# Kernel optimization log

Measured on AMD Instinct MI355X. Metric: run time of the kernel, lower is better.

The kernel has to match this reference:

```python
import jax, jax.numpy as jnp
import numpy as np

T, B, IN_DIM, MEM_DIM = 512, 64, 512, 512


def _kaiming(key, shape):
    fan_in = shape[1]
    return jax.random.normal(key, shape, dtype=jnp.float32) * np.sqrt(2.0 / fan_in)


def setup_inputs() -> dict:
    key = jax.random.key(0)
    ks = jax.random.split(key, 5)
    return {
        "inputs": jax.random.normal(ks[0], (T, B, IN_DIM), dtype=jnp.float32),
        "h0": jnp.zeros((B, MEM_DIM), dtype=jnp.float32),
        "c0": jnp.zeros((B, MEM_DIM), dtype=jnp.float32),
        "W_ioux": _kaiming(ks[1], (3 * MEM_DIM, IN_DIM)),
        "b_ioux": jnp.zeros((3 * MEM_DIM,), dtype=jnp.float32),
        "W_iouh": _kaiming(ks[2], (3 * MEM_DIM, MEM_DIM)),
        "b_iouh": jnp.zeros((3 * MEM_DIM,), dtype=jnp.float32),
        "W_fx": _kaiming(ks[3], (MEM_DIM, IN_DIM)),
        "b_fx": jnp.zeros((MEM_DIM,), dtype=jnp.float32),
        "W_fh": _kaiming(ks[4], (MEM_DIM, MEM_DIM)),
        "b_fh": jnp.zeros((MEM_DIM,), dtype=jnp.float32),
    }


def reference(inputs, h0, c0, W_ioux, b_ioux, W_iouh, b_iouh, W_fx, b_fx, W_fh, b_fh):
    # Precompute input-side projections for all timesteps (one big GEMM each).
    x_iou = jnp.einsum('tbi,gi->tbg', inputs, W_ioux) + b_ioux  # [T,B,3M]
    x_f = jnp.einsum('tbi,mi->tbm', inputs, W_fx) + b_fx        # [T,B,M]

    def step(carry, xt):
        c, h = carry
        xiou_t, xf_t = xt
        iou = xiou_t + h @ W_iouh.T + b_iouh
        i, o, u = jnp.split(iou, 3, axis=-1)
        i = jax.nn.sigmoid(i)
        o = jax.nn.sigmoid(o)
        u = jnp.tanh(u)
        f = jax.nn.sigmoid(xf_t + h @ W_fh.T + b_fh)
        c_new = i * u + f * c
        h_new = o * jnp.tanh(c_new)
        return (c_new, h_new), h_new

    (c_final, h_final), output = jax.lax.scan(step, (c0, h0), (x_iou, x_f))
    # Matches torch: (stacked hidden states [T,B,M], final (c, h))
    return output, c_final, h_final
```

## Files before the change

### kernel.cpp

```cpp
#include <hip/hip_runtime.h>
#include <math.h>

#define T_STEPS 512
#define BATCH   64
#define INDIM   512
#define MEMDIM  512
#define NWG     256
#define NT      1024


#define SMEM_FLOATS (8*1028 + 4*8*68 + 16*8*68 + 2*64 + 8)

extern "C" __global__ void __launch_bounds__(NT, 1)
lstm_scan(const float* __restrict__ inputs, const float* __restrict__ h0,
          const float* __restrict__ c0,
          const float* __restrict__ W_ioux, const float* __restrict__ b_ioux,
          const float* __restrict__ W_iouh, const float* __restrict__ b_iouh,
          const float* __restrict__ W_fx,   const float* __restrict__ b_fx,
          const float* __restrict__ W_fh,   const float* __restrict__ b_fh,
          float* __restrict__ out, int* __restrict__ bar)
{
    extern __shared__ float smem[];
    float* W_s    = smem;
    float* xpart  = smem + 8*1028;
    float* hpart  = xpart + 4*8*68;
    float* c_s    = hpart + 16*8*68;
    float* bias_s = c_s + 2*64;

    float* hist = (float*)(bar + 2048);

    const int tid  = threadIdx.x;
    const int wg   = blockIdx.x;
    const int lane = tid & 63;
    const int wv16 = tid >> 6;

    const int q    = tid >> 8;
    const int r    = tid & 255;
    const int j8   = r & 7;
    const int bsub = (r >> 3) & 7;
    const int wv   = r >> 6;
    const int b0   = 16 * wv + bsub;
    const int b1   = b0 + 8;

    const int s    = lane & 31;
    const int dsub = lane >> 5;

    for (int i = tid; i < 8 * 256; i += NT) {
        int row = i >> 8;
        int c4  = i & 255;
        int mloc = row >> 2, gate = row & 3;
        int mg = 2 * wg + mloc;
        const float* src;
        if (c4 < 128) {
            const float* Wx = (gate < 3) ? (W_ioux + (size_t)(gate * 512 + mg) * INDIM)
                                         : (W_fx   + (size_t)mg * INDIM);
            src = Wx + c4 * 4;
        } else {
            const float* Wh = (gate < 3) ? (W_iouh + (size_t)(gate * 512 + mg) * MEMDIM)
                                         : (W_fh   + (size_t)mg * MEMDIM);
            src = Wh + (c4 - 128) * 4;
        }
        float4 v = *(const float4*)src;
        *(float4*)&W_s[row * 1028 + c4 * 4] = v;
    }
    if (tid < 8) {
        int mloc = tid >> 2, gate = tid & 3, mg = 2 * wg + mloc;
        bias_s[tid] = (gate < 3) ? (b_ioux[gate * 512 + mg] + b_iouh[gate * 512 + mg])
                                 : (b_fx[mg] + b_fh[mg]);
    }
    if (tid < 128) {
        int mloc = tid >> 6, b = tid & 63;
        c_s[mloc * 64 + b] = c0[(size_t)b * MEMDIM + 2 * wg + mloc];
        float hv = h0[(size_t)b * MEMDIM + 2 * wg + mloc];
        __hip_atomic_store(&hist[(2 * wg + mloc) * 64 + b], hv,
                           __ATOMIC_RELAXED, __HIP_MEMORY_SCOPE_AGENT);
    }
    __syncthreads();

    if (tid == 0) {
        __hip_atomic_store(&bar[wg], 1, __ATOMIC_RELAXED, __HIP_MEMORY_SCOPE_AGENT);
    }

    const float4* wrowx = (const float4*)&W_s[j8 * 1028] + q * 32;

    for (int t = 0; t < T_STEPS; ++t) {
        const float4* x0p = (const float4*)(inputs + ((size_t)t * BATCH + b0) * INDIM) + q * 32;
        const float4* x1p = (const float4*)(inputs + ((size_t)t * BATCH + b1) * INDIM) + q * 32;
        float4 a0 = make_float4(0.f, 0.f, 0.f, 0.f);
        float4 a1 = make_float4(0.f, 0.f, 0.f, 0.f);
#pragma unroll 8
        for (int k = 0; k < 32; ++k) {
            float4 w  = wrowx[k];
            float4 v0 = x0p[k];
            float4 v1 = x1p[k];
            a0.x += v0.x * w.x; a0.y += v0.y * w.y; a0.z += v0.z * w.z; a0.w += v0.w * w.w;
            a1.x += v1.x * w.x; a1.y += v1.y * w.y; a1.z += v1.z * w.z; a1.w += v1.w * w.w;
        }
        xpart[q * 544 + j8 * 68 + b0] = a0.x + a0.y + a0.z + a0.w;
        xpart[q * 544 + j8 * 68 + b1] = a1.x + a1.y + a1.z + a1.w;

        if (tid < 64) {
            const unsigned long long* slots = (const unsigned long long*)bar;
            const int need = t + 1;
            for (;;) {
                unsigned long long v0 = __hip_atomic_load(slots + 2 * tid,
                                                          __ATOMIC_RELAXED,
                                                          __HIP_MEMORY_SCOPE_AGENT);
                unsigned long long v1 = __hip_atomic_load(slots + 2 * tid + 1,
                                                          __ATOMIC_RELAXED,
                                                          __HIP_MEMORY_SCOPE_AGENT);
                int e0 = (int)(unsigned)(v0 & 0xffffffffULL);
                int e1 = (int)(unsigned)(v0 >> 32);
                int e2 = (int)(unsigned)(v1 & 0xffffffffULL);
                int e3 = (int)(unsigned)(v1 >> 32);
                int m0 = e0 < e1 ? e0 : e1;
                int m1 = e2 < e3 ? e2 : e3;
                int mn = m0 < m1 ? m0 : m1;
                if (__all(mn >= need)) break;
                __builtin_amdgcn_s_sleep(1);
            }
        }
        __syncthreads();

        const unsigned long long* hrow =
            (const unsigned long long*)(hist + (size_t)(t & 1) * 32768);
        float2 hacc[8];
#pragma unroll
        for (int j = 0; j < 8; ++j) { hacc[j].x = 0.f; hacc[j].y = 0.f; }
#pragma unroll 4
        for (int it = 0; it < 16; ++it) {
            int d = wv16 * 32 + it * 2 + dsub;
            unsigned long long u = __hip_atomic_load(hrow + d * 32 + s,
                                                     __ATOMIC_RELAXED,
                                                     __HIP_MEMORY_SCOPE_AGENT);
            float2 hv = __builtin_bit_cast(float2, u);
#pragma unroll
            for (int j = 0; j < 8; ++j) {
                float wj = W_s[j * 1028 + 512 + d];
                hacc[j].x += wj * hv.x;
                hacc[j].y += wj * hv.y;
            }
        }
#pragma unroll
        for (int j = 0; j < 8; ++j) {
            hacc[j].x += __shfl_xor(hacc[j].x, 32);
            hacc[j].y += __shfl_xor(hacc[j].y, 32);
        }
        if (lane < 32) {
#pragma unroll
            for (int j = 0; j < 8; ++j)
                *(float2*)&hpart[wv16 * 544 + j * 68 + 2 * s] = hacc[j];
        }
        __syncthreads();

        float hn = 0.f, cn = 0.f;
        int mloc = tid >> 6, b = tid & 63;
        if (tid < 128) {
            float g[4];
#pragma unroll
            for (int gi = 0; gi < 4; ++gi) {
                int j = mloc * 4 + gi;
                float v = bias_s[j];
#pragma unroll
                for (int qq = 0; qq < 4; ++qq) v += xpart[qq * 544 + j * 68 + b];
#pragma unroll
                for (int w = 0; w < 16; ++w)  v += hpart[w * 544 + j * 68 + b];
                g[gi] = v;
            }
            float ig = 1.f / (1.f + expf(-g[0]));
            float og = 1.f / (1.f + expf(-g[1]));
            float ug = tanhf(g[2]);
            float fg = 1.f / (1.f + expf(-g[3]));
            cn = ig * ug + fg * c_s[mloc * 64 + b];
            c_s[mloc * 64 + b] = cn;
            hn = og * tanhf(cn);
            __hip_atomic_store(&hist[(size_t)((t + 1) & 1) * 32768
                                     + (2 * wg + mloc) * 64 + b], hn,
                               __ATOMIC_RELAXED, __HIP_MEMORY_SCOPE_AGENT);
        }
        __syncthreads();

        if (tid == 0) {
            __hip_atomic_store(&bar[wg], t + 2, __ATOMIC_RELAXED,
                               __HIP_MEMORY_SCOPE_AGENT);
        }

        if (tid < 128) {
            int mg = 2 * wg + mloc;
            out[((size_t)t * BATCH + b) * MEMDIM + mg] = hn;
            if (t == T_STEPS - 1) {
                out[(size_t)T_STEPS * BATCH * MEMDIM + (size_t)b * MEMDIM + mg] = cn;
                out[(size_t)T_STEPS * BATCH * MEMDIM + (size_t)BATCH * MEMDIM
                    + (size_t)b * MEMDIM + mg] = hn;
            }
        }
    }
}

extern "C" void kernel_launch(void* const* d_in, const int* in_sizes, int n_in,
                              void* d_out, int out_size, void* d_ws, size_t ws_size,
                              hipStream_t stream) {
    (void)in_sizes; (void)n_in; (void)out_size; (void)ws_size;
    const float* inputs = (const float*)d_in[0];
    const float* h0     = (const float*)d_in[1];
    const float* c0     = (const float*)d_in[2];
    const float* W_ioux = (const float*)d_in[3];
    const float* b_ioux = (const float*)d_in[4];
    const float* W_iouh = (const float*)d_in[5];
    const float* b_iouh = (const float*)d_in[6];
    const float* W_fx   = (const float*)d_in[7];
    const float* b_fx   = (const float*)d_in[8];
    const float* W_fh   = (const float*)d_in[9];
    const float* b_fh   = (const float*)d_in[10];
    float* out = (float*)d_out;
    int*   bar = (int*)d_ws;

    const size_t smem_bytes = SMEM_FLOATS * sizeof(float);
    (void)hipFuncSetAttribute((const void*)lstm_scan,
                              hipFuncAttributeMaxDynamicSharedMemorySize,
                              (int)smem_bytes);

    (void)hipMemsetAsync(d_ws, 0, 8192, stream);

    void* args[] = { (void*)&inputs, (void*)&h0, (void*)&c0,
                     (void*)&W_ioux, (void*)&b_ioux, (void*)&W_iouh, (void*)&b_iouh,
                     (void*)&W_fx, (void*)&b_fx, (void*)&W_fh, (void*)&b_fh,
                     (void*)&out, (void*)&bar };

    hipError_t err = hipLaunchCooperativeKernel((const void*)lstm_scan,
                                                dim3(NWG), dim3(NT),
                                                args, smem_bytes, stream);
    if (err != hipSuccess) {
        hipLaunchKernelGGL(lstm_scan, dim3(NWG), dim3(NT), smem_bytes, stream,
                           inputs, h0, c0, W_ioux, b_ioux, W_iouh, b_iouh,
                           W_fx, b_fx, W_fh, b_fh, out, bar);
    }
}
```

Baseline: 6.507 ms.

## Use per-timestep h history ring and per-wave barrier polling to drop block sync

When the workspace is large enough, each timestep's hidden state goes to its own slot in a full-history buffer rather than a double buffer. That lets reads use plain float2 loads instead of atomic loads and removes the write-after-read hazard across steps. The barrier wait is also restructured so every wave polls its own 16 slot flags, which removes the __syncthreads after the wait. The trade-offs are a much larger workspace, more polling traffic from all waves, and relying on plain loads seeing fresh data that was written with relaxed atomics.

```diff
diff --git a/kernel.cpp b/kernel.cpp
--- a/kernel.cpp
+++ b/kernel.cpp
@@ -18,7 +18,7 @@
           const float* __restrict__ W_iouh, const float* __restrict__ b_iouh,
           const float* __restrict__ W_fx,   const float* __restrict__ b_fx,
           const float* __restrict__ W_fh,   const float* __restrict__ b_fh,
-          float* __restrict__ out, int* __restrict__ bar)
+          float* __restrict__ out, int* __restrict__ bar, int ring)
 {
     extern __shared__ float smem[];
     float* W_s    = smem;
@@ -99,46 +99,52 @@
         xpart[q * 544 + j8 * 68 + b0] = a0.x + a0.y + a0.z + a0.w;
         xpart[q * 544 + j8 * 68 + b1] = a1.x + a1.y + a1.z + a1.w;
 
-        if (tid < 64) {
-            const unsigned long long* slots = (const unsigned long long*)bar;
+        {
             const int need = t + 1;
             for (;;) {
-                unsigned long long v0 = __hip_atomic_load(slots + 2 * tid,
-                                                          __ATOMIC_RELAXED,
-                                                          __HIP_MEMORY_SCOPE_AGENT);
-                unsigned long long v1 = __hip_atomic_load(slots + 2 * tid + 1,
-                                                          __ATOMIC_RELAXED,
-                                                          __HIP_MEMORY_SCOPE_AGENT);
-                int e0 = (int)(unsigned)(v0 & 0xffffffffULL);
-                int e1 = (int)(unsigned)(v0 >> 32);
-                int e2 = (int)(unsigned)(v1 & 0xffffffffULL);
-                int e3 = (int)(unsigned)(v1 >> 32);
-                int m0 = e0 < e1 ? e0 : e1;
-                int m1 = e2 < e3 ? e2 : e3;
-                int mn = m0 < m1 ? m0 : m1;
-                if (__all(mn >= need)) break;
+                int e = 0x7fffffff;
+                if (lane < 16)
+                    e = __hip_atomic_load(&bar[wv16 * 16 + lane], __ATOMIC_RELAXED,
+                                          __HIP_MEMORY_SCOPE_AGENT);
+                if (__all(e >= need)) break;
                 __builtin_amdgcn_s_sleep(1);
             }
-        }
-        __syncthreads();
-
-        const unsigned long long* hrow =
-            (const unsigned long long*)(hist + (size_t)(t & 1) * 32768);
+            asm volatile("" ::: "memory");
+        }
+
         float2 hacc[8];
 #pragma unroll
         for (int j = 0; j < 8; ++j) { hacc[j].x = 0.f; hacc[j].y = 0.f; }
+
+        if (ring) {
+            const float* hrow = hist + (size_t)t * 32768;
 #pragma unroll 4
-        for (int it = 0; it < 16; ++it) {
-            int d = wv16 * 32 + it * 2 + dsub;
-            unsigned long long u = __hip_atomic_load(hrow + d * 32 + s,
-                                                     __ATOMIC_RELAXED,
-                                                     __HIP_MEMORY_SCOPE_AGENT);
-            float2 hv = __builtin_bit_cast(float2, u);
-#pragma unroll
-            for (int j = 0; j < 8; ++j) {
-                float wj = W_s[j * 1028 + 512 + d];
-                hacc[j].x += wj * hv.x;
-                hacc[j].y += wj * hv.y;
+            for (int it = 0; it < 16; ++it) {
+                int d = wv16 * 32 + it * 2 + dsub;
+                float2 hv = *(const float2*)(hrow + d * 64 + 2 * s);
+#pragma unroll
+                for (int j = 0; j < 8; ++j) {
+                    float wj = W_s[j * 1028 + 512 + d];
+                    hacc[j].x += wj * hv.x;
+                    hacc[j].y += wj * hv.y;
+                }
+            }
+        } else {
+            const unsigned long long* hrow =
+                (const unsigned long long*)(hist + (size_t)(t & 1) * 32768);
+#pragma unroll 4
+            for (int it = 0; it < 16; ++it) {
+                int d = wv16 * 32 + it * 2 + dsub;
+                unsigned long long u = __hip_atomic_load(hrow + d * 32 + s,
+                                                         __ATOMIC_RELAXED,
+                                                         __HIP_MEMORY_SCOPE_AGENT);
+                float2 hv = __builtin_bit_cast(float2, u);
+#pragma unroll
+                for (int j = 0; j < 8; ++j) {
+                    float wj = W_s[j * 1028 + 512 + d];
+                    hacc[j].x += wj * hv.x;
+                    hacc[j].y += wj * hv.y;
+                }
             }
         }
 #pragma unroll
@@ -174,8 +180,8 @@
             cn = ig * ug + fg * c_s[mloc * 64 + b];
             c_s[mloc * 64 + b] = cn;
             hn = og * tanhf(cn);
-            __hip_atomic_store(&hist[(size_t)((t + 1) & 1) * 32768
-                                     + (2 * wg + mloc) * 64 + b], hn,
+            size_t wroff = ring ? (size_t)(t + 1) * 32768 : (size_t)((t + 1) & 1) * 32768;
+            __hip_atomic_store(&hist[wroff + (2 * wg + mloc) * 64 + b], hn,
                                __ATOMIC_RELAXED, __HIP_MEMORY_SCOPE_AGENT);
         }
         __syncthreads();
@@ -200,7 +206,7 @@
 extern "C" void kernel_launch(void* const* d_in, const int* in_sizes, int n_in,
                               void* d_out, int out_size, void* d_ws, size_t ws_size,
                               hipStream_t stream) {
-    (void)in_sizes; (void)n_in; (void)out_size; (void)ws_size;
+    (void)in_sizes; (void)n_in; (void)out_size;
     const float* inputs = (const float*)d_in[0];
     const float* h0     = (const float*)d_in[1];
     const float* c0     = (const float*)d_in[2];
@@ -215,6 +221,9 @@
     float* out = (float*)d_out;
     int*   bar = (int*)d_ws;
 
+    const size_t need_ring = 8192 + (size_t)513 * 32768 * 4;
+    int ring = (ws_size >= need_ring) ? 1 : 0;
+
     const size_t smem_bytes = SMEM_FLOATS * sizeof(float);
     (void)hipFuncSetAttribute((const void*)lstm_scan,
                               hipFuncAttributeMaxDynamicSharedMemorySize,
@@ -225,7 +234,7 @@
     void* args[] = { (void*)&inputs, (void*)&h0, (void*)&c0,
                      (void*)&W_ioux, (void*)&b_ioux, (void*)&W_iouh, (void*)&b_iouh,
                      (void*)&W_fx, (void*)&b_fx, (void*)&W_fh, (void*)&b_fh,
-                     (void*)&out, (void*)&bar };
+                     (void*)&out, (void*)&bar, (void*)&ring };
 
     hipError_t err = hipLaunchCooperativeKernel((const void*)lstm_scan,
                                                 dim3(NWG), dim3(NT),
@@ -233,6 +242,6 @@
     if (err != hipSuccess) {
         hipLaunchKernelGGL(lstm_scan, dim3(NWG), dim3(NT), smem_bytes, stream,
                            inputs, h0, c0, W_ioux, b_ioux, W_iouh, b_iouh,
-                           W_fx, b_fx, W_fh, b_fh, out, bar);
+                           W_fx, b_fx, W_fh, b_fh, out, bar, ring);
     }
 }
```

Result: faster. 6.269 ms (-3.7%).
